# Kernel tuning notes

Hardware: AMD Instinct MI355X
Metric: run time of the kernel (lower is better)

## Reference

```python
import jax, jax.numpy as jnp
import numpy as np

B, S, D = 2, 2048, 4096
H, ROT = 16, 64
HD = D // H  # 256


def rotate_every_two(x):
    # x: (..., d) with d even; interleave (-x_odd, x_even)
    x1 = x[..., ::2]
    x2 = x[..., 1::2]
    return jnp.stack((-x2, x1), axis=-1).reshape(x.shape)


def setup_inputs() -> dict:
    key = jax.random.key(0)
    ks = jax.random.split(key, 8)
    hidden_states = jax.random.normal(ks[0], (B, S, D), dtype=jnp.float32)
    # GPT-J style repeat-interleaved sin/cos over rotary_dim, broadcast over heads
    inv_freq = 1.0 / (10000.0 ** (jnp.arange(0, ROT, 2, dtype=jnp.float32) / ROT))
    t = jnp.arange(S, dtype=jnp.float32)
    freqs = jnp.einsum('s,f->sf', t, inv_freq)                    # (S, ROT/2)
    freqs = jnp.repeat(freqs, 2, axis=-1)                         # (S, ROT)
    sin = jnp.sin(freqs)[None, :, None, :]                        # (1, S, 1, ROT)
    cos = jnp.cos(freqs)[None, :, None, :]
    scale = 0.02
    Wq = jax.random.normal(ks[1], (D, D), dtype=jnp.float32) * scale
    Wk = jax.random.normal(ks[2], (D, D), dtype=jnp.float32) * scale
    Wv = jax.random.normal(ks[3], (D, D), dtype=jnp.float32) * scale
    Wo = jax.random.normal(ks[4], (D, D), dtype=jnp.float32) * scale
    return {"hidden_states": hidden_states, "sin": sin, "cos": cos,
            "Wq": Wq, "Wk": Wk, "Wv": Wv, "Wo": Wo}


def reference(hidden_states, sin, cos, Wq, Wk, Wv, Wo):
    b, s, d = hidden_states.shape
    # projections (nn.Linear, no bias): y = x @ W.T
    q = (hidden_states @ Wq.T).reshape(b, s, H, HD)
    k = (hidden_states @ Wk.T).reshape(b, s, H, HD)
    v = (hidden_states @ Wv.T).reshape(b, s, H, HD)

    def rope(x):
        x_rot, x_pass = x[..., :ROT], x[..., ROT:]
        x_rot = x_rot * cos + rotate_every_two(x_rot) * sin
        return jnp.concatenate([x_rot, x_pass], axis=-1)

    q = rope(q).transpose(0, 2, 1, 3)  # (B, H, S, HD)
    k = rope(k).transpose(0, 2, 1, 3)
    v = v.transpose(0, 2, 1, 3)

    inv_scale = 1.0 / np.sqrt(HD).astype(np.float32)
    scores = jnp.einsum('bhqd,bhkd->bhqk', q, k) * inv_scale      # (B, H, S, S)
    # scaled_masked_triangular_softmax == causal masked softmax
    causal = jnp.tril(jnp.ones((s, s), dtype=bool))
    scores = jnp.where(causal[None, None], scores, jnp.finfo(scores.dtype).min)
    attn = jax.nn.softmax(scores, axis=-1)
    out = jnp.einsum('bhqk,bhkd->bhqd', attn, v)                  # (B, H, S, HD)
    out = out.transpose(0, 2, 1, 3).reshape(b, s, d)              # merge heads
    return out @ Wo.T
```

## Files before the change

kernel.cpp:

```cpp
#include <hip/hip_runtime.h>
#include <cstdint>
#include <cstddef>

#define TB 2
#define TS 2048
#define TD 4096
#define TH 16
#define THD 256
#define TROT 64
#define TM (TB*TS)

typedef __attribute__((ext_vector_type(8))) short bf16x8;
typedef __attribute__((ext_vector_type(4))) float f32x4;

#define LGKM0  asm volatile("s_waitcnt lgkmcnt(0)" ::: "memory")
#define VMCNT8 asm volatile("s_waitcnt vmcnt(8)" ::: "memory")
#define VMCNT4 asm volatile("s_waitcnt vmcnt(4)" ::: "memory")
#define VMCNT0 asm volatile("s_waitcnt vmcnt(0)" ::: "memory")
#define SBAR   __builtin_amdgcn_s_barrier()
#define SCHED0 __builtin_amdgcn_sched_barrier(0)
#define PRIO1  __builtin_amdgcn_s_setprio(1)
#define PRIO0  __builtin_amdgcn_s_setprio(0)

__device__ __forceinline__ unsigned short f2bf(float f) {
  union { float f; unsigned u; } v; v.f = f;
  return (unsigned short)((v.u + 0x7fffu + ((v.u >> 16) & 1u)) >> 16);
}

__device__ __forceinline__ void gld16(const void* g, void* l) {
  __builtin_amdgcn_global_load_lds(
      (const __attribute__((address_space(1))) unsigned int*)g,
      (__attribute__((address_space(3))) unsigned int*)l, 16, 0, 0);
}

__global__ __launch_bounds__(256) void k_cvt5(
    const float* __restrict__ s0, const float* __restrict__ s1,
    const float* __restrict__ s2, const float* __restrict__ s3,
    const float* __restrict__ s4, unsigned short* __restrict__ dst) {
  int i = blockIdx.x * 256 + threadIdx.x;
  int tsel = i >> 22, il = i & 4194303;
  const float* s = tsel == 0 ? s0 : tsel == 1 ? s1 : tsel == 2 ? s2 : tsel == 3 ? s3 : s4;
  float4 v = reinterpret_cast<const float4*>(s)[il];
  ushort4 o;
  o.x = f2bf(v.x); o.y = f2bf(v.y); o.z = f2bf(v.z); o.w = f2bf(v.w);
  *reinterpret_cast<ushort4*>(dst + (size_t)i * 4) = o;
}

#define GSTG(SBUF, SAB, SHALF, SKOFS) { \
    const unsigned short* _s = (SAB) ? srcB : srcA; \
    const int _b = (SBUF)*32768 + (SAB)*16384 + (SHALF)*8192; \
    gld16(_s + (size_t)(SHALF)*128*TD + (SKOFS) + roff[0], &lds[_b + t*8]); \
    gld16(_s + (size_t)(SHALF)*128*TD + (SKOFS) + roff[1], &lds[_b + (512+t)*8]); }

#define GLD_AF(DST, BUF, QA) { \
    _Pragma("unroll") for (int m = 0; m < 4; ++m) \
    _Pragma("unroll") for (int kk = 0; kk < 2; ++kk) \
      DST[m][kk] = *(const bf16x8*)&lds[(BUF)*32768 + (QA)*8192 + ((wm*4+m)*2+kk)*512 + llo]; }

#define GLD_BQ(DST, BUF, QB) { \
    _Pragma("unroll") for (int n = 0; n < 2; ++n) \
    _Pragma("unroll") for (int kk = 0; kk < 2; ++kk) \
      DST[n][kk] = *(const bf16x8*)&lds[(BUF)*32768 + 16384 + (QB)*8192 + ((wn*2+n)*2+kk)*512 + llo]; }

#define GMF(AF, BQ, QA, QB) { \
    _Pragma("unroll") for (int kk = 0; kk < 2; ++kk) \
    _Pragma("unroll") for (int m = 0; m < 4; ++m) \
    _Pragma("unroll") for (int n = 0; n < 2; ++n) \
      acc[QA][QB][m][n] = __builtin_amdgcn_mfma_f32_16x16x32_bf16( \
          AF[m][kk], BQ[n][kk], acc[QA][QB][m][n], 0,0,0); }

#define GEMM_MAIN_LOOP \
  GSTG(0,0,0, 0);  SCHED0; \
  GSTG(0,1,0, 0);  SCHED0; \
  GSTG(0,0,1, 0);  SCHED0; \
  GSTG(0,1,1, 0);  SCHED0; \
  GSTG(1,0,0, 64); SCHED0; \
  GSTG(1,1,0, 64); SCHED0; \
  VMCNT4; SBAR; SCHED0; \
  for (int i2 = 0; i2 < NT/2; ++i2) { \
    const int k1c = (2*i2+1) * 64; \
    const int k0n = (2*i2+2 < NT ? 2*i2+2 : NT-1) * 64; \
    const int k1n = (2*i2+3 < NT ? 2*i2+3 : NT-1) * 64; \
    GLD_AF(afP, 0, 0); GLD_BQ(bqP, 0, 0); \
    GSTG(1,0,1, k1c); \
    SBAR; LGKM0; SCHED0; \
    PRIO1; GLD_BQ(bqQ, 0, 1); GMF(afP, bqP, 0, 0); PRIO0; \
    SBAR; SCHED0; \
    GSTG(1,1,1, k1c); \
    SBAR; LGKM0; SCHED0; \
    PRIO1; GLD_AF(afQ, 0, 1); GMF(afP, bqQ, 0, 1); PRIO0; \
    SBAR; SCHED0; \
    GSTG(0,0,0, k0n); \
    SBAR; LGKM0; SCHED0; \
    PRIO1; GMF(afQ, bqP, 1, 0); PRIO0; \
    SBAR; SCHED0; \
    GSTG(0,1,0, k0n); \
    VMCNT4; \
    SBAR; LGKM0; SCHED0; \
    PRIO1; GMF(afQ, bqQ, 1, 1); PRIO0; \
    SBAR; SCHED0; \
    GLD_AF(afP, 1, 0); GLD_BQ(bqP, 1, 0); \
    GSTG(0,0,1, k0n); \
    SBAR; LGKM0; SCHED0; \
    PRIO1; GLD_BQ(bqQ, 1, 1); GMF(afP, bqP, 0, 0); PRIO0; \
    SBAR; SCHED0; \
    GSTG(0,1,1, k0n); \
    SBAR; LGKM0; SCHED0; \
    PRIO1; GLD_AF(afQ, 1, 1); GMF(afP, bqQ, 0, 1); PRIO0; \
    SBAR; SCHED0; \
    GSTG(1,0,0, k1n); \
    SBAR; LGKM0; SCHED0; \
    PRIO1; GMF(afQ, bqP, 1, 0); PRIO0; \
    SBAR; SCHED0; \
    GSTG(1,1,0, k1n); \
    VMCNT4; \
    SBAR; LGKM0; SCHED0; \
    PRIO1; GMF(afQ, bqQ, 1, 1); PRIO0; \
    SBAR; SCHED0; \
  }

#define GEMM_PREAMBLE \
  const int K = TD; \
  const int t = threadIdx.x; \
  const int w = t >> 6, l = t & 63, lr = l & 15, lh = l >> 4; \
  const int wm = w >> 2, wn = w & 3; \
  const int llo = lr * 32 + ((lh ^ ((lr >> 1) & 3)) * 8); \
  int roff[2]; \
  _Pragma("unroll") \
  for (int it = 0; it < 2; ++it) { \
    int c = it * 512 + t; \
    int rl = (c >> 2) & 15; \
    roff[it] = (16 * (c >> 7) + rl) * K + ((c >> 6) & 1) * 32 + ((c & 3) ^ ((rl >> 1) & 3)) * 8; \
  } \
  f32x4 acc[2][2][4][2]; \
  _Pragma("unroll") \
  for (int qa = 0; qa < 2; ++qa) \
  _Pragma("unroll") \
    for (int qb = 0; qb < 2; ++qb) \
  _Pragma("unroll") \
      for (int m = 0; m < 4; ++m) \
  _Pragma("unroll") \
        for (int n = 0; n < 2; ++n) acc[qa][qb][m][n] = 0.f; \
  bf16x8 afP[4][2], afQ[4][2], bqP[2][2], bqQ[2][2]; \
  const int NT = K / 64;

__global__ __launch_bounds__(512, 1) void k_gqkv(
    const unsigned short* __restrict__ A, const unsigned short* __restrict__ W,
    unsigned short* __restrict__ Qo, unsigned short* __restrict__ Ko,
    unsigned short* __restrict__ Vo,
    const float* __restrict__ sinp, const float* __restrict__ cosp)
{
  extern __shared__ unsigned short lds[];
  const int id = blockIdx.x;
  const int swz = (id & 7) * 96 + (id >> 3);
  const int m0 = (swz / 48) * 256, n0 = (swz % 48) * 256;

  GEMM_PREAMBLE
  const unsigned short* srcA = A + (size_t)m0 * K;
  const unsigned short* srcB = W + (size_t)n0 * K;

  GEMM_MAIN_LOOP

  VMCNT0;
  const int tsel = n0 >> 12;
  if (tsel == 2) {
    SBAR;
    const int n0v = n0 - 8192;
    const int b = m0 >> 11, sbase = m0 & (TS - 1);
#pragma unroll
    for (int qb = 0; qb < 2; ++qb)
#pragma unroll
      for (int n = 0; n < 2; ++n) {
        __syncthreads();
#pragma unroll
        for (int qa = 0; qa < 2; ++qa)
#pragma unroll
          for (int m = 0; m < 4; ++m) {
            int lcol = wn * 16 + lr;
            int srow = qa * 128 + wm * 64 + m * 16 + lh * 4;
            ushort4 o;
            o.x = f2bf(acc[qa][qb][m][n][0]); o.y = f2bf(acc[qa][qb][m][n][1]);
            o.z = f2bf(acc[qa][qb][m][n][2]); o.w = f2bf(acc[qa][qb][m][n][3]);
            *(ushort4*)&lds[lcol * 268 + srow] = o;
          }
        __syncthreads();
#pragma unroll
        for (int rr = 0; rr < 4; ++rr) {
          int idx = rr * 512 + t;
          int dl = idx >> 5, sc = (idx & 31) * 8;
          uint4 v = *(const uint4*)&lds[dl * 268 + sc];
          int d = n0v + qb * 128 + (dl >> 4) * 32 + n * 16 + (dl & 15);
          *(uint4*)(Vo + ((size_t)((b * TH + (d >> 8)) * THD + (d & 255))) * TS + sbase + sc) = v;
        }
      }
  } else {
    unsigned short* outp = tsel ? Ko : Qo;
    const int nbase = n0 & 4095;
#pragma unroll
    for (int qa = 0; qa < 2; ++qa)
#pragma unroll
      for (int qb = 0; qb < 2; ++qb)
#pragma unroll
        for (int m = 0; m < 4; ++m)
#pragma unroll
          for (int n = 0; n < 2; ++n)
#pragma unroll
            for (int r = 0; r < 4; ++r) {
              int row = m0 + qa * 128 + wm * 64 + m * 16 + lh * 4 + r;
              int col = nbase + qb * 128 + wn * 32 + n * 16 + lr;
              float x = acc[qa][qb][m][n][r];
              float part = __shfl_xor(x, 1, 64);
              int s = row & (TS - 1), b = row >> 11;
              int h = col >> 8, d = col & 255;
              float val = x;
              if (d < TROT) {
                float cc = cosp[s * TROT + d], ss = sinp[s * TROT + d];
                val = x * cc + ((d & 1) ? part : -part) * ss;
              }
              outp[((size_t)(b * TH + h) * TS + s) * THD + d] = f2bf(val);
            }
  }
}

__global__ __launch_bounds__(512, 1) void k_gout(
    const unsigned short* __restrict__ A, const unsigned short* __restrict__ W,
    float* __restrict__ out)
{
  extern __shared__ unsigned short lds[];
  const int id = blockIdx.x;
  const int swz = (id & 7) * 32 + (id >> 3);
  const int m0 = (swz >> 4) * 256, n0 = (swz & 15) * 256;

  GEMM_PREAMBLE
  const unsigned short* srcA = A + (size_t)m0 * K;
  const unsigned short* srcB = W + (size_t)n0 * K;

  GEMM_MAIN_LOOP

  VMCNT0;
#pragma unroll
  for (int qa = 0; qa < 2; ++qa)
#pragma unroll
    for (int qb = 0; qb < 2; ++qb)
#pragma unroll
      for (int m = 0; m < 4; ++m)
#pragma unroll
        for (int n = 0; n < 2; ++n)
#pragma unroll
          for (int r = 0; r < 4; ++r) {
            int row = m0 + qa * 128 + wm * 64 + m * 16 + lh * 4 + r;
            int col = n0 + qb * 128 + wn * 32 + n * 16 + lr;
            out[(size_t)row * TD + col] = acc[qa][qb][m][n][r];
          }
}

__global__ __launch_bounds__(256, 2) void k_fattn(
    const unsigned short* __restrict__ Qt, const unsigned short* __restrict__ Kt,
    const unsigned short* __restrict__ Vt, unsigned short* __restrict__ O)
{
  extern __shared__ unsigned short sh[];
  const int t = threadIdx.x, w = t >> 6, l = t & 63, lr = l & 15, lh = l >> 4;
  const int bh = blockIdx.x;
  const int qb = (gridDim.y - 1) - blockIdx.y;
  const int q0 = qb * 64;
  const int jmax = qb;

  const unsigned short* kbase = Kt + (size_t)bh * TS * THD;
  const unsigned short* vbase = Vt + (size_t)bh * THD * TS;

  const int llo = lr * 32 + ((lh ^ ((lr >> 1) & 3)) * 8);

  int koff[8], voff[8];
#pragma unroll
  for (int it = 0; it < 8; ++it) {
    int c = it * 256 + t;
    int row = (c >> 2) & 15;
    int scc = (c & 3) ^ ((row >> 1) & 3);
    koff[it] = (((c >> 9) & 3) * 16 + row) * THD + ((c >> 6) & 7) * 32 + scc * 8;
    voff[it] = (((c >> 6) & 15) * 16 + row) * TS + ((c >> 10) & 1) * 32 + scc * 8;
  }

  bf16x8 qf[8];
  const unsigned short* qp = Qt + ((size_t)bh * TS + q0 + w * 16 + lr) * THD;
#pragma unroll
  for (int kk = 0; kk < 8; ++kk) qf[kk] = *(const bf16x8*)(qp + kk * 32 + lh * 8);

  f32x4 oacc[16];
#pragma unroll
  for (int i = 0; i < 16; ++i) oacc[i] = 0.f;
  float mrow[4] = {-__builtin_inff(), -__builtin_inff(), -__builtin_inff(), -__builtin_inff()};
  float lrow[4] = {0.f, 0.f, 0.f, 0.f};

#pragma unroll
  for (int it = 0; it < 8; ++it) gld16(kbase + koff[it], &sh[(it*256 + t) * 8]);
#pragma unroll
  for (int it = 0; it < 8; ++it) gld16(vbase + voff[it], &sh[16384 + (it*256 + t) * 8]);

  for (int j = 0; j <= jmax; ++j) {
    const bool nx = (j < jmax);
    VMCNT8; SBAR; SCHED0;

    f32x4 sacc[4];
#pragma unroll
    for (int nt = 0; nt < 4; ++nt) sacc[nt] = 0.f;
    PRIO1;
#pragma unroll
    for (int kk = 0; kk < 8; ++kk)
#pragma unroll
      for (int nt = 0; nt < 4; ++nt) {
        bf16x8 kf = *(const bf16x8*)&sh[(nt*8 + kk)*512 + llo];
        sacc[nt] = __builtin_amdgcn_mfma_f32_16x16x32_bf16(qf[kk], kf, sacc[nt], 0, 0, 0);
      }
    PRIO0;
    LGKM0; SBAR; SCHED0;
    if (nx) {
      const unsigned short* kj = kbase + (size_t)(j + 1) * 64 * THD;
#pragma unroll
      for (int it = 0; it < 8; ++it) gld16(kj + koff[it], &sh[(it*256 + t) * 8]);
    }

    float p[4][4];
    const int qrow0 = q0 + w * 16 + lh * 4;
#pragma unroll
    for (int nt = 0; nt < 4; ++nt) {
      int kpos = j * 64 + nt * 16 + lr;
#pragma unroll
      for (int r = 0; r < 4; ++r) {
        float sv = sacc[nt][r] * 0.0625f;
        if (kpos > qrow0 + r) sv = -__builtin_inff();
        p[nt][r] = sv;
      }
    }
    float lmax[4];
#pragma unroll
    for (int r = 0; r < 4; ++r)
      lmax[r] = fmaxf(fmaxf(p[0][r], p[1][r]), fmaxf(p[2][r], p[3][r]));
    float g = fmaxf(fmaxf(lmax[0] - mrow[0], lmax[1] - mrow[1]),
                    fmaxf(lmax[2] - mrow[2], lmax[3] - mrow[3]));
    if (__any(g > 8.f)) {
      float tmax[4] = {lmax[0], lmax[1], lmax[2], lmax[3]};
#pragma unroll
      for (int off = 1; off < 16; off <<= 1)
#pragma unroll
        for (int r = 0; r < 4; ++r) tmax[r] = fmaxf(tmax[r], __shfl_xor(tmax[r], off, 64));
      float alpha[4];
#pragma unroll
      for (int r = 0; r < 4; ++r) {
        float mn = fmaxf(mrow[r], tmax[r]);
        alpha[r] = __expf(mrow[r] - mn);
        mrow[r] = mn;
        lrow[r] *= alpha[r];
      }
#pragma unroll
      for (int i = 0; i < 16; ++i)
#pragma unroll
        for (int r = 0; r < 4; ++r) oacc[i][r] *= alpha[r];
    }
#pragma unroll
    for (int r = 0; r < 4; ++r) {
      float pe0 = __expf(p[0][r] - mrow[r]);
      float pe1 = __expf(p[1][r] - mrow[r]);
      float pe2 = __expf(p[2][r] - mrow[r]);
      float pe3 = __expf(p[3][r] - mrow[r]);
      p[0][r] = pe0; p[1][r] = pe1; p[2][r] = pe2; p[3][r] = pe3;
      lrow[r] += (pe0 + pe1) + (pe2 + pe3);
    }

    const int wb = 32768 + w * 1152;
#pragma unroll
    for (int nt = 0; nt < 4; ++nt)
#pragma unroll
      for (int r = 0; r < 4; ++r)
        sh[wb + (lh*4 + r)*72 + nt*16 + lr] = f2bf(p[nt][r]);
    bf16x8 pfr0 = *(const bf16x8*)&sh[wb + lr*72 + lh*8];
    bf16x8 pfr1 = *(const bf16x8*)&sh[wb + lr*72 + 32 + lh*8];

    if (nx) { VMCNT8; } else { VMCNT0; }
    SBAR; SCHED0;
    PRIO1;
#pragma unroll
    for (int dt = 0; dt < 16; ++dt) {
      bf16x8 vf = *(const bf16x8*)&sh[16384 + dt*512 + llo];
      oacc[dt] = __builtin_amdgcn_mfma_f32_16x16x32_bf16(pfr0, vf, oacc[dt], 0, 0, 0);
    }
#pragma unroll
    for (int dt = 0; dt < 16; ++dt) {
      bf16x8 vf = *(const bf16x8*)&sh[16384 + (16 + dt)*512 + llo];
      oacc[dt] = __builtin_amdgcn_mfma_f32_16x16x32_bf16(pfr1, vf, oacc[dt], 0, 0, 0);
    }
    PRIO0;
    LGKM0; SBAR; SCHED0;
    if (nx) {
      const unsigned short* vj = vbase + (size_t)(j + 1) * 64;
#pragma unroll
      for (int it = 0; it < 8; ++it) gld16(vj + voff[it], &sh[16384 + (it*256 + t) * 8]);
    }
  }

#pragma unroll
  for (int off = 1; off < 16; off <<= 1)
#pragma unroll
    for (int r = 0; r < 4; ++r) lrow[r] += __shfl_xor(lrow[r], off, 64);

  const int b = bh >> 4, h = bh & 15;
  float inv[4];
#pragma unroll
  for (int r = 0; r < 4; ++r) inv[r] = 1.f / lrow[r];
#pragma unroll
  for (int dt = 0; dt < 16; ++dt)
#pragma unroll
    for (int r = 0; r < 4; ++r) {
      int s = q0 + w * 16 + lh * 4 + r;
      O[((size_t)(b * TS + s) * TH + h) * THD + dt * 16 + lr] = f2bf(oacc[dt][r] * inv[r]);
    }
}

extern "C" void kernel_launch(void* const* d_in, const int* in_sizes, int n_in,
                              void* d_out, int out_size, void* d_ws, size_t ws_size,
                              hipStream_t stream) {
  const float* hs   = (const float*)d_in[0];
  const float* sinp = (const float*)d_in[1];
  const float* cosp = (const float*)d_in[2];
  const float* Wq   = (const float*)d_in[3];
  const float* Wk   = (const float*)d_in[4];
  const float* Wv   = (const float*)d_in[5];
  const float* Wo   = (const float*)d_in[6];

  const size_t NE = (size_t)TM * TD;
  const size_t BYTES = NE * 2;
  char* ws = (char*)d_ws;
  unsigned short* hsb = (unsigned short*)(ws + 0*BYTES);
  unsigned short* Wqb = (unsigned short*)(ws + 1*BYTES);
  unsigned short* Wob = (unsigned short*)(ws + 4*BYTES);
  unsigned short* Qt  = (unsigned short*)(ws + 5*BYTES);
  unsigned short* Ktb = (unsigned short*)(ws + 6*BYTES);
  unsigned short* Vtb = (unsigned short*)(ws + 7*BYTES);
  unsigned short* Ob  = (unsigned short*)(ws + 8*BYTES);

  k_cvt5<<<81920, 256, 0, stream>>>(hs, Wq, Wk, Wv, Wo, hsb);

  k_gqkv<<<768, 512, 131072, stream>>>(hsb, Wqb, Qt, Ktb, Vtb, sinp, cosp);

  k_fattn<<<dim3(TB*TH, TS/64), 256, 74752, stream>>>(Qt, Ktb, Vtb, Ob);

  k_gout<<<256, 512, 131072, stream>>>(Ob, Wob, (float*)d_out);
}
```

Before: 699.8 us.

## Switch projection GEMMs to 32x32x16 MFMA with matching LDS layout

The QKV and output projection GEMMs move from 16x16x32 bf16 MFMA to 32x32x16 bf16 MFMA. The global-to-LDS staging offsets, LDS fragment reads and epilogues are rewritten to match the 32x32 accumulator layout. This uses fewer, larger MFMA instructions and fewer LDS fragment loads per k-step. The new LDS layout drops the XOR swizzle, which risks more LDS bank conflicts. The V-transpose epilogue now uses one LDS pass per 128-column half instead of two.

```diff
diff --git a/kernel.cpp b/kernel.cpp
--- a/kernel.cpp
+++ b/kernel.cpp
@@ -12,6 +12,7 @@
 
 typedef __attribute__((ext_vector_type(8))) short bf16x8;
 typedef __attribute__((ext_vector_type(4))) float f32x4;
+typedef __attribute__((ext_vector_type(16))) float f32x16;
 
 #define LGKM0  asm volatile("s_waitcnt lgkmcnt(0)" ::: "memory")
 #define VMCNT8 asm volatile("s_waitcnt vmcnt(8)" ::: "memory")
@@ -53,21 +54,19 @@
     gld16(_s + (size_t)(SHALF)*128*TD + (SKOFS) + roff[1], &lds[_b + (512+t)*8]); }
 
 #define GLD_AF(DST, BUF, QA) { \
-    _Pragma("unroll") for (int m = 0; m < 4; ++m) \
-    _Pragma("unroll") for (int kk = 0; kk < 2; ++kk) \
-      DST[m][kk] = *(const bf16x8*)&lds[(BUF)*32768 + (QA)*8192 + ((wm*4+m)*2+kk)*512 + llo]; }
+    _Pragma("unroll") for (int mt = 0; mt < 2; ++mt) \
+    _Pragma("unroll") for (int kc = 0; kc < 4; ++kc) \
+      DST[mt][kc] = *(const bf16x8*)&lds[(BUF)*32768 + (QA)*8192 + ((wm*2+mt)*4+kc)*512 + llo]; }
 
 #define GLD_BQ(DST, BUF, QB) { \
-    _Pragma("unroll") for (int n = 0; n < 2; ++n) \
-    _Pragma("unroll") for (int kk = 0; kk < 2; ++kk) \
-      DST[n][kk] = *(const bf16x8*)&lds[(BUF)*32768 + 16384 + (QB)*8192 + ((wn*2+n)*2+kk)*512 + llo]; }
+    _Pragma("unroll") for (int kc = 0; kc < 4; ++kc) \
+      DST[kc] = *(const bf16x8*)&lds[(BUF)*32768 + 16384 + (QB)*8192 + (wn*4+kc)*512 + llo]; }
 
 #define GMF(AF, BQ, QA, QB) { \
-    _Pragma("unroll") for (int kk = 0; kk < 2; ++kk) \
-    _Pragma("unroll") for (int m = 0; m < 4; ++m) \
-    _Pragma("unroll") for (int n = 0; n < 2; ++n) \
-      acc[QA][QB][m][n] = __builtin_amdgcn_mfma_f32_16x16x32_bf16( \
-          AF[m][kk], BQ[n][kk], acc[QA][QB][m][n], 0,0,0); }
+    _Pragma("unroll") for (int kc = 0; kc < 4; ++kc) \
+    _Pragma("unroll") for (int mt = 0; mt < 2; ++mt) \
+      acc[QA][QB][mt] = __builtin_amdgcn_mfma_f32_32x32x16_bf16( \
+          AF[mt][kc], BQ[kc], acc[QA][QB][mt], 0,0,0); }
 
 #define GEMM_MAIN_LOOP \
   GSTG(0,0,0, 0);  SCHED0; \
@@ -122,26 +121,27 @@
 #define GEMM_PREAMBLE \
   const int K = TD; \
   const int t = threadIdx.x; \
-  const int w = t >> 6, l = t & 63, lr = l & 15, lh = l >> 4; \
+  const int w = t >> 6, l = t & 63; \
   const int wm = w >> 2, wn = w & 3; \
-  const int llo = lr * 32 + ((lh ^ ((lr >> 1) & 3)) * 8); \
+  const int llo = (l & 31) * 16 + (l >> 5) * 8; \
   int roff[2]; \
   _Pragma("unroll") \
   for (int it = 0; it < 2; ++it) { \
     int c = it * 512 + t; \
-    int rl = (c >> 2) & 15; \
-    roff[it] = (16 * (c >> 7) + rl) * K + ((c >> 6) & 1) * 32 + ((c & 3) ^ ((rl >> 1) & 3)) * 8; \
+    int g_row = ((c >> 8) & 3) * 32 + ((c >> 1) & 31); \
+    int g_k   = ((c >> 6) & 3) * 16 + (c & 1) * 8; \
+    roff[it] = g_row * K + g_k; \
   } \
-  f32x4 acc[2][2][4][2]; \
+  f32x16 acc[2][2][2]; \
   _Pragma("unroll") \
   for (int qa = 0; qa < 2; ++qa) \
   _Pragma("unroll") \
     for (int qb = 0; qb < 2; ++qb) \
   _Pragma("unroll") \
-      for (int m = 0; m < 4; ++m) \
+      for (int mt = 0; mt < 2; ++mt) \
   _Pragma("unroll") \
-        for (int n = 0; n < 2; ++n) acc[qa][qb][m][n] = 0.f; \
-  bf16x8 afP[4][2], afQ[4][2], bqP[2][2], bqQ[2][2]; \
+        for (int e = 0; e < 16; ++e) acc[qa][qb][mt][e] = 0.f; \
+  bf16x8 afP[2][4], afQ[2][4], bqP[4], bqQ[4]; \
   const int NT = K / 64;
 
 __global__ __launch_bounds__(512, 1) void k_gqkv(
@@ -168,31 +168,33 @@
     const int n0v = n0 - 8192;
     const int b = m0 >> 11, sbase = m0 & (TS - 1);
 #pragma unroll
-    for (int qb = 0; qb < 2; ++qb)
-#pragma unroll
-      for (int n = 0; n < 2; ++n) {
-        __syncthreads();
-#pragma unroll
-        for (int qa = 0; qa < 2; ++qa)
-#pragma unroll
-          for (int m = 0; m < 4; ++m) {
-            int lcol = wn * 16 + lr;
-            int srow = qa * 128 + wm * 64 + m * 16 + lh * 4;
+    for (int qb = 0; qb < 2; ++qb) {
+      __syncthreads();
+#pragma unroll
+      for (int qa = 0; qa < 2; ++qa)
+#pragma unroll
+        for (int mt = 0; mt < 2; ++mt) {
+          int colL = wn * 32 + (l & 31);
+          int rb0 = qa * 128 + wm * 64 + mt * 32 + 4 * (l >> 5);
+          f32x16 a = acc[qa][qb][mt];
+#pragma unroll
+          for (int q = 0; q < 4; ++q) {
             ushort4 o;
-            o.x = f2bf(acc[qa][qb][m][n][0]); o.y = f2bf(acc[qa][qb][m][n][1]);
-            o.z = f2bf(acc[qa][qb][m][n][2]); o.w = f2bf(acc[qa][qb][m][n][3]);
-            *(ushort4*)&lds[lcol * 268 + srow] = o;
+            o.x = f2bf(a[4*q]);   o.y = f2bf(a[4*q+1]);
+            o.z = f2bf(a[4*q+2]); o.w = f2bf(a[4*q+3]);
+            *(ushort4*)&lds[colL * 264 + rb0 + 8 * q] = o;
           }
-        __syncthreads();
-#pragma unroll
-        for (int rr = 0; rr < 4; ++rr) {
-          int idx = rr * 512 + t;
-          int dl = idx >> 5, sc = (idx & 31) * 8;
-          uint4 v = *(const uint4*)&lds[dl * 268 + sc];
-          int d = n0v + qb * 128 + (dl >> 4) * 32 + n * 16 + (dl & 15);
-          *(uint4*)(Vo + ((size_t)((b * TH + (d >> 8)) * THD + (d & 255))) * TS + sbase + sc) = v;
         }
+      __syncthreads();
+#pragma unroll
+      for (int rr = 0; rr < 8; ++rr) {
+        int idx = rr * 512 + t;
+        int dl = idx >> 5, sc = idx & 31;
+        uint4 v = *(const uint4*)&lds[dl * 264 + sc * 8];
+        int d = n0v + qb * 128 + dl;
+        *(uint4*)(Vo + ((size_t)((b * TH + (d >> 8)) * THD + (d & 255))) * TS + sbase + sc * 8) = v;
       }
+    }
   } else {
     unsigned short* outp = tsel ? Ko : Qo;
     const int nbase = n0 & 4095;
@@ -201,24 +203,25 @@
 #pragma unroll
       for (int qb = 0; qb < 2; ++qb)
 #pragma unroll
-        for (int m = 0; m < 4; ++m)
-#pragma unroll
-          for (int n = 0; n < 2; ++n)
-#pragma unroll
-            for (int r = 0; r < 4; ++r) {
-              int row = m0 + qa * 128 + wm * 64 + m * 16 + lh * 4 + r;
-              int col = nbase + qb * 128 + wn * 32 + n * 16 + lr;
-              float x = acc[qa][qb][m][n][r];
-              float part = __shfl_xor(x, 1, 64);
-              int s = row & (TS - 1), b = row >> 11;
-              int h = col >> 8, d = col & 255;
-              float val = x;
-              if (d < TROT) {
-                float cc = cosp[s * TROT + d], ss = sinp[s * TROT + d];
-                val = x * cc + ((d & 1) ? part : -part) * ss;
-              }
-              outp[((size_t)(b * TH + h) * TS + s) * THD + d] = f2bf(val);
+        for (int mt = 0; mt < 2; ++mt) {
+          f32x16 a = acc[qa][qb][mt];
+          int col = nbase + qb * 128 + wn * 32 + (l & 31);
+          int h = col >> 8, d = col & 255;
+          int rowb = m0 + qa * 128 + wm * 64 + mt * 32 + 4 * (l >> 5);
+#pragma unroll
+          for (int reg = 0; reg < 16; ++reg) {
+            int row = rowb + (reg & 3) + 8 * (reg >> 2);
+            float x = a[reg];
+            float part = __shfl_xor(x, 1, 64);
+            int s = row & (TS - 1), bb = row >> 11;
+            float val = x;
+            if (d < TROT) {
+              float cc = cosp[s * TROT + d], ss = sinp[s * TROT + d];
+              val = x * cc + ((d & 1) ? part : -part) * ss;
             }
+            outp[((size_t)(bb * TH + h) * TS + s) * THD + d] = f2bf(val);
+          }
+        }
   }
 }
 
@@ -243,15 +246,14 @@
 #pragma unroll
     for (int qb = 0; qb < 2; ++qb)
 #pragma unroll
-      for (int m = 0; m < 4; ++m)
-#pragma unroll
-        for (int n = 0; n < 2; ++n)
-#pragma unroll
-          for (int r = 0; r < 4; ++r) {
-            int row = m0 + qa * 128 + wm * 64 + m * 16 + lh * 4 + r;
-            int col = n0 + qb * 128 + wn * 32 + n * 16 + lr;
-            out[(size_t)row * TD + col] = acc[qa][qb][m][n][r];
-          }
+      for (int mt = 0; mt < 2; ++mt) {
+        f32x16 a = acc[qa][qb][mt];
+        int col = n0 + qb * 128 + wn * 32 + (l & 31);
+        int rowb = m0 + qa * 128 + wm * 64 + mt * 32 + 4 * (l >> 5);
+#pragma unroll
+        for (int reg = 0; reg < 16; ++reg)
+          out[(size_t)(rowb + (reg & 3) + 8 * (reg >> 2)) * TD + col] = a[reg];
+      }
 }
 
 __global__ __launch_bounds__(256, 2) void k_fattn(
```

Result: slower. 785.3 us (+12.2%).
